# Kernel tuning notes

Measured on AMD Instinct MI355X. Metric: run time of the kernel, lower is better.

## Reference

```python
import jax, jax.numpy as jnp
import numpy as np


def setup_inputs() -> dict:
    key = jax.random.key(0)
    k1, k2, k3 = jax.random.split(key, 3)
    B, R, Din, D = 4096, 4096, 1024, 1024
    x = jax.random.normal(k1, (B, Din), dtype=jnp.float32)
    refs = jax.random.normal(k2, (R, Din), dtype=jnp.float32)
    W = jax.random.normal(k3, (Din, D), dtype=jnp.float32) * (1.0 / np.sqrt(Din))
    b = jnp.zeros((D,), dtype=jnp.float32)
    return {"x": x, "refs": refs, "W": W, "b": b}


def reference(x, refs, W, b) -> jnp.ndarray:
    # feature extractor (linear stand-in for the CResNet embedding)
    vin = x @ W + b          # (B, D)
    vrefs = refs @ W + b     # (R, D)
    # compute_degradation_metric: mean_r ||vin_b - vref_r||^2
    # = ||vin||^2 + mean_r ||vref_r||^2 - 2 * vin @ mean_r(vref_r)
    # Same math as the naive broadcast-sub-square-sum-mean, GEMM-friendly form.
    sq_in = jnp.sum(vin * vin, axis=1)                 # (B,)
    mean_sq_ref = jnp.mean(jnp.sum(vrefs * vrefs, axis=1))  # scalar
    mean_ref = jnp.mean(vrefs, axis=0)                 # (D,)
    cross = vin @ mean_ref                             # (B,)
    degradation_metric = sq_in + mean_sq_ref - 2.0 * cross
    return degradation_metric
```

## Files before the change

kernel.cpp:

```cpp
#include <hip/hip_runtime.h>
#include <hip/hip_bf16.h>
#include <stdint.h>


typedef __attribute__((ext_vector_type(8))) short short8;
typedef __attribute__((ext_vector_type(4))) float f32x4;

__device__ __forceinline__ short f2bf(float f) {
  uint32_t u = __builtin_bit_cast(uint32_t, f);
  uint32_t r = (u + 0x7fffu + ((u >> 16) & 1u)) >> 16;
  return (short)r;
}
__device__ __forceinline__ float bf2f(short s) {
  uint32_t u = ((uint32_t)(uint16_t)s) << 16;
  return __builtin_bit_cast(float, u);
}

#define WS_WT 16777216u
#define WS_CP 18874368u
#define WS_CS 20971520u
#define WS_XP 20979712u
#define WS_RR 20996096u

__global__ __launch_bounds__(256) void k_prep(
    const float* __restrict__ refs, const float* __restrict__ W,
    short* __restrict__ wt, float* __restrict__ cspart, float* __restrict__ zacc) {
  __shared__ short tile[64][68];
  const int b = blockIdx.x, t = threadIdx.x;
  if (b < 512) {
    const int rblk = b;
    const int c0 = t * 4;
    float s0 = 0.f, s1 = 0.f, s2 = 0.f, s3 = 0.f;
    for (int r = rblk * 8; r < rblk * 8 + 8; ++r) {
      float4 v = *(const float4*)&refs[(size_t)r * 1024 + c0];
      s0 += v.x; s1 += v.y; s2 += v.z; s3 += v.w;
    }
    cspart[rblk * 1024 + c0 + 0] = s0;
    cspart[rblk * 1024 + c0 + 1] = s1;
    cspart[rblk * 1024 + c0 + 2] = s2;
    cspart[rblk * 1024 + c0 + 3] = s3;
  } else if (b < 768) {
    const int tb = b - 512;
    const int tk = (tb >> 4) * 64, tn = (tb & 15) * 64;
    const int kk = t >> 4, nn4 = (t & 15) * 4;
#pragma unroll
    for (int p = 0; p < 4; ++p) {
      int k = kk + p * 16;
      float4 v = *(const float4*)&W[(size_t)(tk + k) * 1024 + tn + nn4];
      tile[nn4 + 0][k] = f2bf(v.x);
      tile[nn4 + 1][k] = f2bf(v.y);
      tile[nn4 + 2][k] = f2bf(v.z);
      tile[nn4 + 3][k] = f2bf(v.w);
    }
    __syncthreads();
    const int nn = t >> 4, kk4 = (t & 15) * 4;
#pragma unroll
    for (int p = 0; p < 4; ++p) {
      int n = nn + p * 16;
      uint32_t lo = (uint16_t)tile[n][kk4 + 0] | ((uint32_t)(uint16_t)tile[n][kk4 + 1] << 16);
      uint32_t hi = (uint16_t)tile[n][kk4 + 2] | ((uint32_t)(uint16_t)tile[n][kk4 + 3] << 16);
      *(uint2*)&wt[(size_t)(tn + n) * 1024 + tk + kk4] = make_uint2(lo, hi);
    }
  } else {
    const int i = (b - 768) * 256 + t;
    ((float4*)zacc)[i]        = make_float4(0.f, 0.f, 0.f, 0.f);
    ((float4*)zacc)[i + 1024] = make_float4(0.f, 0.f, 0.f, 0.f);
  }
}

__global__ void k_colsum(const float* __restrict__ cspart, float* __restrict__ colsum) {
  __shared__ float sh[8][32];
  const int t = threadIdx.x;
  const int c = t & 31, pg = t >> 5;
  const int k = blockIdx.x * 32 + c;
  float s = 0.f;
  for (int i = 0; i < 64; ++i) s += cspart[(size_t)(pg * 64 + i) * 1024 + k];
  sh[pg][c] = s;
  __syncthreads();
  if (t < 32) {
    float tot = 0.f;
#pragma unroll
    for (int g = 0; g < 8; ++g) tot += sh[g][t];
    colsum[blockIdx.x * 32 + t] = tot;
  }
}

__global__ __launch_bounds__(512, 4) void k_main(
    const float* __restrict__ X, const float* __restrict__ R,
    const short* __restrict__ Wt, const float* __restrict__ bias,
    const float* __restrict__ colsum, float* __restrict__ xpart,
    float* __restrict__ refrow) {
  __shared__ __align__(16) short As[2][128 * 64];
  __shared__ __align__(16) short Bs[2][128 * 64];
  __shared__ __align__(16) short cs_lds[1024];
  const int t = threadIdx.x;
  const int w = t >> 6, l = t & 63;
  const int wr = w >> 2, wc = w & 3;
  const int bx = blockIdx.x;
  const int nt = bx >> 6;
  const int mt = bx & 63;
  const bool is_x = (mt < 32);
  const float* Am = is_x ? X : R;
  const int m0 = (is_x ? mt : (mt - 32)) * 128;
  const int n0 = nt * 128;

  const int srow = t >> 3;
  const int sslot = t & 7;
  const int arow = t >> 4;
  const int acol = (t & 15) * 4;
  const int asl = (t & 15) >> 1, ah = t & 1;

  f32x4 acc[4][2] = {};
  f32x4 acc_t[2] = {};
  float4 areg[4];

  auto stageB = [&](int buf, int kt) {
    const int k0 = kt * 64;
#pragma unroll
    for (int issue = 0; issue < 2; ++issue) {
      const int row = srow + issue * 64;
      const int sg = sslot ^ (row & 7);
      const short* gb = Wt + ((size_t)(n0 + row) * 1024 + k0 + sg * 8);
      char* lb = (char*)&Bs[buf][0] + issue * 8192 + w * 1024;
      __builtin_amdgcn_global_load_lds(
          (const __attribute__((address_space(1))) unsigned int*)gb,
          (__attribute__((address_space(3))) unsigned int*)lb, 16, 0, 0);
    }
  };
  auto loadA = [&](int kt) {
    const int k0 = kt * 64;
#pragma unroll
    for (int i = 0; i < 4; ++i) {
      const int r = arow + i * 32;
      areg[i] = *(const float4*)&Am[(size_t)(m0 + r) * 1024 + k0 + acol];
    }
  };
  auto writeA = [&](int buf) {
#pragma unroll
    for (int i = 0; i < 4; ++i) {
      const int r = arow + i * 32;
      uint32_t lo, hi;
      asm("v_cvt_pk_bf16_f32 %0, %1, %2" : "=v"(lo) : "v"(areg[i].x), "v"(areg[i].y));
      asm("v_cvt_pk_bf16_f32 %0, %1, %2" : "=v"(hi) : "v"(areg[i].z), "v"(areg[i].w));
      char* p = (char*)&As[buf][0] + r * 128 + (((asl ^ (r & 7)) * 16) + ah * 8);
      *(uint2*)p = make_uint2(lo, hi);
    }
  };

  loadA(0);
  stageB(0, 0);
  stageB(1, 1);
  writeA(0);
  loadA(1);
  if (is_x && t < 128) {
    float4 c0 = *(const float4*)&colsum[t * 8];
    float4 c1 = *(const float4*)&colsum[t * 8 + 4];
    uint32_t p0, p1, p2, p3;
    asm("v_cvt_pk_bf16_f32 %0, %1, %2" : "=v"(p0) : "v"(c0.x), "v"(c0.y));
    asm("v_cvt_pk_bf16_f32 %0, %1, %2" : "=v"(p1) : "v"(c0.z), "v"(c0.w));
    asm("v_cvt_pk_bf16_f32 %0, %1, %2" : "=v"(p2) : "v"(c1.x), "v"(c1.y));
    asm("v_cvt_pk_bf16_f32 %0, %1, %2" : "=v"(p3) : "v"(c1.z), "v"(c1.w));
    *(uint4*)&cs_lds[t * 8] = make_uint4(p0, p1, p2, p3);
  }

  for (int kt = 0; kt < 16; ++kt) {
    if (kt < 15) asm volatile("s_waitcnt vmcnt(6) lgkmcnt(0)" ::: "memory");
    else         asm volatile("s_waitcnt vmcnt(0) lgkmcnt(0)" ::: "memory");
    __builtin_amdgcn_s_barrier();
    const int cur = kt & 1;
    if (kt + 1 < 16) writeA((kt + 1) & 1);
    if (kt + 2 < 16) loadA(kt + 2);
#pragma unroll
    for (int kk = 0; kk < 2; ++kk) {
      short8 af[4], bfr[2];
#pragma unroll
      for (int i = 0; i < 4; ++i) {
        const int ra = wr * 64 + i * 16 + (l & 15);
        const int s = (l >> 4) + kk * 4;
        af[i] = *(const short8*)&As[cur][ra * 64 + ((s ^ (ra & 7)) * 8)];
      }
#pragma unroll
      for (int j = 0; j < 2; ++j) {
        const int rbw = wc * 32 + j * 16 + (l & 15);
        const int s = (l >> 4) + kk * 4;
        bfr[j] = *(const short8*)&Bs[cur][rbw * 64 + ((s ^ (rbw & 7)) * 8)];
      }
      __builtin_amdgcn_s_setprio(1);
#pragma unroll
      for (int i = 0; i < 4; ++i)
#pragma unroll
        for (int j = 0; j < 2; ++j)
          acc[i][j] = __builtin_amdgcn_mfma_f32_16x16x32_bf16(af[i], bfr[j], acc[i][j], 0, 0, 0);
      if (is_x && wr == 0) {
        short8 csf = *(const short8*)&cs_lds[kt * 64 + kk * 32 + (l >> 4) * 8];
#pragma unroll
        for (int j = 0; j < 2; ++j)
          acc_t[j] = __builtin_amdgcn_mfma_f32_16x16x32_bf16(csf, bfr[j], acc_t[j], 0, 0, 0);
      }
      __builtin_amdgcn_s_setprio(0);
    }
    __builtin_amdgcn_s_barrier();
    if (kt + 2 < 16) stageB(cur, kt + 2);
  }

  float* tpan = (float*)cs_lds;
  if (is_x) {
    if (wr == 0 && l < 16) {
      tpan[wc * 32 + l]      = acc_t[0][0];
      tpan[wc * 32 + 16 + l] = acc_t[1][0];
    }
    __syncthreads();
  }

  float bv[2], tvv[2];
#pragma unroll
  for (int n2 = 0; n2 < 2; ++n2) {
    const int ci = wc * 32 + n2 * 16 + (l & 15);
    bv[n2] = bias[n0 + ci];
    tvv[n2] = is_x ? (tpan[ci] * (1.0f / 4096.0f) + bv[n2]) : 0.f;
  }
#pragma unroll
  for (int m4 = 0; m4 < 4; ++m4) {
#pragma unroll
    for (int j = 0; j < 4; ++j) {
      if (is_x) {
        float sq = 0.f, cr = 0.f;
#pragma unroll
        for (int n2 = 0; n2 < 2; ++n2) {
          const float v = acc[m4][n2][j] + bv[n2];
          sq += v * v;
          cr += v * tvv[n2];
        }
        float comb = sq - 2.0f * cr;
#pragma unroll
        for (int off = 1; off < 16; off <<= 1) comb += __shfl_xor(comb, off, 64);
        if ((l & 15) == 0) {
          const int rm = m0 + wr * 64 + m4 * 16 + (l >> 4) * 4 + j;
          atomicAdd(&xpart[rm], comb);
        }
      } else {
        float sq = 0.f;
#pragma unroll
        for (int n2 = 0; n2 < 2; ++n2) {
          const float v = acc[m4][n2][j] + bv[n2];
          sq += v * v;
        }
#pragma unroll
        for (int off = 1; off < 16; off <<= 1) sq += __shfl_xor(sq, off, 64);
        if ((l & 15) == 0) {
          const int rm = m0 + wr * 64 + m4 * 16 + (l >> 4) * 4 + j;
          atomicAdd(&refrow[rm], sq);
        }
      }
    }
  }
}

__global__ void k_tail(const float* __restrict__ refrow, const float* __restrict__ xpart,
                       float* __restrict__ out) {
  __shared__ float sh[16];
  const int t = threadIdx.x;
  float s = 0.f;
  for (int i = t; i < 4096; i += 1024) s += refrow[i];
#pragma unroll
  for (int off = 32; off; off >>= 1) s += __shfl_down(s, off, 64);
  const int w = t >> 6, l = t & 63;
  if (l == 0) sh[w] = s;
  __syncthreads();
  if (t == 0) {
    float tot = 0.f;
#pragma unroll
    for (int i = 0; i < 16; ++i) tot += sh[i];
    sh[0] = tot * (1.0f / 4096.0f);
  }
  __syncthreads();
  const float ms = sh[0];
  for (int i = t; i < 4096; i += 1024) out[i] = xpart[i] + ms;
}

extern "C" void kernel_launch(void* const* d_in, const int* in_sizes, int n_in,
                              void* d_out, int out_size, void* d_ws, size_t ws_size,
                              hipStream_t stream) {
  const float* x    = (const float*)d_in[0];
  const float* refs = (const float*)d_in[1];
  const float* W    = (const float*)d_in[2];
  const float* bias = (const float*)d_in[3];
  float* out = (float*)d_out;
  char* ws = (char*)d_ws;

  short* wt     = (short*)(ws + WS_WT);
  float* cspart = (float*)(ws + WS_CP);
  float* colsum = (float*)(ws + WS_CS);
  float* xpart  = (float*)(ws + WS_XP);
  float* refrow = (float*)(ws + WS_RR);

  hipLaunchKernelGGL(k_prep, dim3(772), dim3(256), 0, stream, refs, W, wt, cspart, xpart);
  hipLaunchKernelGGL(k_colsum, dim3(32), dim3(256), 0, stream, cspart, colsum);
  hipLaunchKernelGGL(k_main, dim3(512), dim3(512), 0, stream, x, refs, wt, bias, colsum, xpart, refrow);
  hipLaunchKernelGGL(k_tail, dim3(1), dim3(1024), 0, stream, refrow, xpart, out);
}
```

Measured before the change: 44.57 us.

## Derive mean reference embedding from refs GEMM, split into two templated GEMM launches

Drops the separate column-sum pass over refs and the bf16 MFMA trick for the mean. The mean of vrefs now comes from the refs GEMM accumulators, reduced per column with atomics into tcol. The single mixed GEMM becomes two launches, refs first and then x. The x launch adds one extra block that folds the mean squared norm into the output with atomics, replacing the tail kernel, and output zeroing moves into the prep kernel. This removes two small kernels and a full refs read, at the cost of serializing the two GEMM halves (256 blocks each instead of 512 at once) and extra atomics.

Result: slower. 51.54 us (+15.6%).

```diff
diff --git a/kernel.cpp b/kernel.cpp
--- a/kernel.cpp
+++ b/kernel.cpp
@@ -11,37 +11,18 @@
   uint32_t r = (u + 0x7fffu + ((u >> 16) & 1u)) >> 16;
   return (short)r;
 }
-__device__ __forceinline__ float bf2f(short s) {
-  uint32_t u = ((uint32_t)(uint16_t)s) << 16;
-  return __builtin_bit_cast(float, u);
-}
-
-#define WS_WT 16777216u
-#define WS_CP 18874368u
-#define WS_CS 20971520u
-#define WS_XP 20979712u
-#define WS_RR 20996096u
+
+#define WS_WT 0u
+#define WS_TC 2097152u
+#define WS_RR 2101248u
 
 __global__ __launch_bounds__(256) void k_prep(
-    const float* __restrict__ refs, const float* __restrict__ W,
-    short* __restrict__ wt, float* __restrict__ cspart, float* __restrict__ zacc) {
+    const float* __restrict__ W, short* __restrict__ wt,
+    float* __restrict__ tcol, float* __restrict__ refrow, float* __restrict__ out) {
   __shared__ short tile[64][68];
   const int b = blockIdx.x, t = threadIdx.x;
-  if (b < 512) {
-    const int rblk = b;
-    const int c0 = t * 4;
-    float s0 = 0.f, s1 = 0.f, s2 = 0.f, s3 = 0.f;
-    for (int r = rblk * 8; r < rblk * 8 + 8; ++r) {
-      float4 v = *(const float4*)&refs[(size_t)r * 1024 + c0];
-      s0 += v.x; s1 += v.y; s2 += v.z; s3 += v.w;
-    }
-    cspart[rblk * 1024 + c0 + 0] = s0;
-    cspart[rblk * 1024 + c0 + 1] = s1;
-    cspart[rblk * 1024 + c0 + 2] = s2;
-    cspart[rblk * 1024 + c0 + 3] = s3;
-  } else if (b < 768) {
-    const int tb = b - 512;
-    const int tk = (tb >> 4) * 64, tn = (tb & 15) * 64;
+  if (b < 256) {
+    const int tk = (b >> 4) * 64, tn = (b & 15) * 64;
     const int kk = t >> 4, nn4 = (t & 15) * 4;
 #pragma unroll
     for (int p = 0; p < 4; ++p) {
@@ -62,46 +43,49 @@
       *(uint2*)&wt[(size_t)(tn + n) * 1024 + tk + kk4] = make_uint2(lo, hi);
     }
   } else {
-    const int i = (b - 768) * 256 + t;
-    ((float4*)zacc)[i]        = make_float4(0.f, 0.f, 0.f, 0.f);
-    ((float4*)zacc)[i + 1024] = make_float4(0.f, 0.f, 0.f, 0.f);
-  }
-}
-
-__global__ void k_colsum(const float* __restrict__ cspart, float* __restrict__ colsum) {
-  __shared__ float sh[8][32];
-  const int t = threadIdx.x;
-  const int c = t & 31, pg = t >> 5;
-  const int k = blockIdx.x * 32 + c;
-  float s = 0.f;
-  for (int i = 0; i < 64; ++i) s += cspart[(size_t)(pg * 64 + i) * 1024 + k];
-  sh[pg][c] = s;
-  __syncthreads();
-  if (t < 32) {
-    float tot = 0.f;
-#pragma unroll
-    for (int g = 0; g < 8; ++g) tot += sh[g][t];
-    colsum[blockIdx.x * 32 + t] = tot;
-  }
-}
-
-__global__ __launch_bounds__(512, 4) void k_main(
-    const float* __restrict__ X, const float* __restrict__ R,
-    const short* __restrict__ Wt, const float* __restrict__ bias,
-    const float* __restrict__ colsum, float* __restrict__ xpart,
-    float* __restrict__ refrow) {
+    const int i = (b - 256) * 256 + t;
+    const float4 z = make_float4(0.f, 0.f, 0.f, 0.f);
+    ((float4*)out)[i] = z;
+    ((float4*)refrow)[i] = z;
+    if (i < 256) ((float4*)tcol)[i] = z;
+  }
+}
+
+template <bool IS_X>
+__global__ __launch_bounds__(512, 4) void k_gemm(
+    const float* __restrict__ Am, const short* __restrict__ Wt,
+    const float* __restrict__ bias, float* __restrict__ tcol,
+    float* __restrict__ refrow, float* __restrict__ out) {
   __shared__ __align__(16) short As[2][128 * 64];
   __shared__ __align__(16) short Bs[2][128 * 64];
-  __shared__ __align__(16) short cs_lds[1024];
   const int t = threadIdx.x;
   const int w = t >> 6, l = t & 63;
+
+  if (IS_X && blockIdx.x >= 256) {
+    __shared__ float sh[8];
+    float s = 0.f;
+    for (int i = t; i < 4096; i += 512) s += refrow[i];
+#pragma unroll
+    for (int off = 32; off; off >>= 1) s += __shfl_down(s, off, 64);
+    if (l == 0) sh[w] = s;
+    __syncthreads();
+    if (t == 0) {
+      float tot = 0.f;
+#pragma unroll
+      for (int i = 0; i < 8; ++i) tot += sh[i];
+      sh[0] = tot * (1.0f / 4096.0f);
+    }
+    __syncthreads();
+    const float ms = sh[0];
+    for (int i = t; i < 4096; i += 512) atomicAdd(&out[i], ms);
+    return;
+  }
+
   const int wr = w >> 2, wc = w & 3;
   const int bx = blockIdx.x;
-  const int nt = bx >> 6;
-  const int mt = bx & 63;
-  const bool is_x = (mt < 32);
-  const float* Am = is_x ? X : R;
-  const int m0 = (is_x ? mt : (mt - 32)) * 128;
+  const int mt = bx & 31;
+  const int nt = bx >> 5;
+  const int m0 = mt * 128;
   const int n0 = nt * 128;
 
   const int srow = t >> 3;
@@ -111,7 +95,6 @@
   const int asl = (t & 15) >> 1, ah = t & 1;
 
   f32x4 acc[4][2] = {};
-  f32x4 acc_t[2] = {};
   float4 areg[4];
 
   auto stageB = [&](int buf, int kt) {
@@ -152,16 +135,6 @@
   stageB(1, 1);
   writeA(0);
   loadA(1);
-  if (is_x && t < 128) {
-    float4 c0 = *(const float4*)&colsum[t * 8];
-    float4 c1 = *(const float4*)&colsum[t * 8 + 4];
-    uint32_t p0, p1, p2, p3;
-    asm("v_cvt_pk_bf16_f32 %0, %1, %2" : "=v"(p0) : "v"(c0.x), "v"(c0.y));
-    asm("v_cvt_pk_bf16_f32 %0, %1, %2" : "=v"(p1) : "v"(c0.z), "v"(c0.w));
-    asm("v_cvt_pk_bf16_f32 %0, %1, %2" : "=v"(p2) : "v"(c1.x), "v"(c1.y));
-    asm("v_cvt_pk_bf16_f32 %0, %1, %2" : "=v"(p3) : "v"(c1.z), "v"(c1.w));
-    *(uint4*)&cs_lds[t * 8] = make_uint4(p0, p1, p2, p3);
-  }
 
   for (int kt = 0; kt < 16; ++kt) {
     if (kt < 15) asm volatile("s_waitcnt vmcnt(6) lgkmcnt(0)" ::: "memory");
@@ -191,39 +164,25 @@
 #pragma unroll
         for (int j = 0; j < 2; ++j)
           acc[i][j] = __builtin_amdgcn_mfma_f32_16x16x32_bf16(af[i], bfr[j], acc[i][j], 0, 0, 0);
-      if (is_x && wr == 0) {
-        short8 csf = *(const short8*)&cs_lds[kt * 64 + kk * 32 + (l >> 4) * 8];
-#pragma unroll
-        for (int j = 0; j < 2; ++j)
-          acc_t[j] = __builtin_amdgcn_mfma_f32_16x16x32_bf16(csf, bfr[j], acc_t[j], 0, 0, 0);
-      }
       __builtin_amdgcn_s_setprio(0);
     }
     __builtin_amdgcn_s_barrier();
     if (kt + 2 < 16) stageB(cur, kt + 2);
   }
 
-  float* tpan = (float*)cs_lds;
-  if (is_x) {
-    if (wr == 0 && l < 16) {
-      tpan[wc * 32 + l]      = acc_t[0][0];
-      tpan[wc * 32 + 16 + l] = acc_t[1][0];
-    }
-    __syncthreads();
-  }
-
-  float bv[2], tvv[2];
-#pragma unroll
-  for (int n2 = 0; n2 < 2; ++n2) {
-    const int ci = wc * 32 + n2 * 16 + (l & 15);
-    bv[n2] = bias[n0 + ci];
-    tvv[n2] = is_x ? (tpan[ci] * (1.0f / 4096.0f) + bv[n2]) : 0.f;
-  }
-#pragma unroll
-  for (int m4 = 0; m4 < 4; ++m4) {
-#pragma unroll
-    for (int j = 0; j < 4; ++j) {
-      if (is_x) {
+  float bv[2];
+#pragma unroll
+  for (int n2 = 0; n2 < 2; ++n2) bv[n2] = bias[n0 + wc * 32 + n2 * 16 + (l & 15)];
+
+  if (IS_X) {
+    float tvv[2];
+#pragma unroll
+    for (int n2 = 0; n2 < 2; ++n2)
+      tvv[n2] = tcol[n0 + wc * 32 + n2 * 16 + (l & 15)] * (1.0f / 4096.0f);
+#pragma unroll
+    for (int m4 = 0; m4 < 4; ++m4) {
+#pragma unroll
+      for (int j = 0; j < 4; ++j) {
         float sq = 0.f, cr = 0.f;
 #pragma unroll
         for (int n2 = 0; n2 < 2; ++n2) {
@@ -236,9 +195,15 @@
         for (int off = 1; off < 16; off <<= 1) comb += __shfl_xor(comb, off, 64);
         if ((l & 15) == 0) {
           const int rm = m0 + wr * 64 + m4 * 16 + (l >> 4) * 4 + j;
-          atomicAdd(&xpart[rm], comb);
-        }
-      } else {
+          atomicAdd(&out[rm], comb);
+        }
+      }
+    }
+  } else {
+#pragma unroll
+    for (int m4 = 0; m4 < 4; ++m4) {
+#pragma unroll
+      for (int j = 0; j < 4; ++j) {
         float sq = 0.f;
 #pragma unroll
         for (int n2 = 0; n2 < 2; ++n2) {
@@ -253,29 +218,19 @@
         }
       }
     }
-  }
-}
-
-__global__ void k_tail(const float* __restrict__ refrow, const float* __restrict__ xpart,
-                       float* __restrict__ out) {
-  __shared__ float sh[16];
-  const int t = threadIdx.x;
-  float s = 0.f;
-  for (int i = t; i < 4096; i += 1024) s += refrow[i];
-#pragma unroll
-  for (int off = 32; off; off >>= 1) s += __shfl_down(s, off, 64);
-  const int w = t >> 6, l = t & 63;
-  if (l == 0) sh[w] = s;
-  __syncthreads();
-  if (t == 0) {
-    float tot = 0.f;
-#pragma unroll
-    for (int i = 0; i < 16; ++i) tot += sh[i];
-    sh[0] = tot * (1.0f / 4096.0f);
-  }
-  __syncthreads();
-  const float ms = sh[0];
-  for (int i = t; i < 4096; i += 1024) out[i] = xpart[i] + ms;
+#pragma unroll
+    for (int n2 = 0; n2 < 2; ++n2) {
+      float cs = 16.0f * bv[n2];
+#pragma unroll
+      for (int m4 = 0; m4 < 4; ++m4)
+#pragma unroll
+        for (int j = 0; j < 4; ++j) cs += acc[m4][n2][j];
+      cs += __shfl_xor(cs, 16, 64);
+      cs += __shfl_xor(cs, 32, 64);
+      if ((l >> 4) == 0)
+        atomicAdd(&tcol[n0 + wc * 32 + n2 * 16 + (l & 15)], cs);
+    }
+  }
 }
 
 extern "C" void kernel_launch(void* const* d_in, const int* in_sizes, int n_in,
@@ -289,13 +244,12 @@
   char* ws = (char*)d_ws;
 
   short* wt     = (short*)(ws + WS_WT);
-  float* cspart = (float*)(ws + WS_CP);
-  float* colsum = (float*)(ws + WS_CS);
-  float* xpart  = (float*)(ws + WS_XP);
+  float* tcol   = (float*)(ws + WS_TC);
   float* refrow = (float*)(ws + WS_RR);
 
-  hipLaunchKernelGGL(k_prep, dim3(772), dim3(256), 0, stream, refs, W, wt, cspart, xpart);
-  hipLaunchKernelGGL(k_colsum, dim3(32), dim3(256), 0, stream, cspart, colsum);
-  hipLaunchKernelGGL(k_main, dim3(512), dim3(512), 0, stream, x, refs, wt, bias, colsum, xpart, refrow);
-  hipLaunchKernelGGL(k_tail, dim3(1), dim3(1024), 0, stream, refrow, xpart, out);
-}
+  hipLaunchKernelGGL(k_prep, dim3(260), dim3(256), 0, stream, W, wt, tcol, refrow, out);
+  hipLaunchKernelGGL(k_gemm<false>, dim3(256), dim3(512), 0, stream,
+                     refs, wt, bias, tcol, refrow, out);
+  hipLaunchKernelGGL(k_gemm<true>, dim3(257), dim3(512), 0, stream,
+                     x, wt, bias, tcol, refrow, out);
+}
```
